# Kernel tuning notes

Measured on AMD Instinct MI355X. Metric: run time of the kernel, lower is better.

## Reference

```python
import jax, jax.numpy as jnp
import numpy as np

B, N, T, N_IN = 4, 40, 64, 4
N_EMB, N_HID = 32, 64
EPS = 1e-05


def _spatial_rels(n):
    # fully-connected directed edges without self-loops (NRI convention)
    offdiag = np.ones((n, n)) - np.eye(n)
    recv_idx, send_idx = np.where(offdiag)[0], np.where(offdiag)[1]
    eye = np.eye(n, dtype=np.float32)
    return eye[recv_idx], eye[send_idx]  # [n*(n-1), n] each


def _temporal_rels(t):
    # all t*t ordered pairs (including self), one-hot
    eye = np.eye(t, dtype=np.float32)
    recv = np.repeat(np.arange(t), t)
    send = np.tile(np.arange(t), t)
    return eye[recv], eye[send]  # [t*t, t] each


def setup_inputs() -> dict:
    key = jax.random.key(0)
    ks = jax.random.split(key, 8)
    rel_rec, rel_send = _spatial_rels(N)
    rel_rec_t, rel_send_t = _temporal_rels(T)
    s_emb = 1.0 / np.sqrt(N_IN)
    s_lstm = 1.0 / np.sqrt(N_HID)
    s_att = 1.0 / np.sqrt(2 * N_HID)
    return {
        "inputs": jax.random.normal(ks[0], (B, N, T, N_IN), dtype=jnp.float32),
        "rel_rec": jnp.asarray(rel_rec),
        "rel_send": jnp.asarray(rel_send),
        "rel_rec_t": jnp.asarray(rel_rec_t),
        "rel_send_t": jnp.asarray(rel_send_t),
        "W_emb": jax.random.uniform(ks[1], (N_EMB, N_IN), jnp.float32, -s_emb, s_emb),
        "b_emb": jnp.zeros((N_EMB,), jnp.float32),
        "W_ih": jax.random.uniform(ks[2], (4 * N_HID, N_EMB), jnp.float32, -s_lstm, s_lstm),
        "W_hh": jax.random.uniform(ks[3], (4 * N_HID, N_HID), jnp.float32, -s_lstm, s_lstm),
        "b_ih": jax.random.uniform(ks[4], (4 * N_HID,), jnp.float32, -s_lstm, s_lstm),
        "b_hh": jax.random.uniform(ks[5], (4 * N_HID,), jnp.float32, -s_lstm, s_lstm),
        "W_att": jax.random.uniform(ks[6], (1, 2 * N_HID), jnp.float32, -s_att, s_att),
        "b_att": jnp.zeros((1,), jnp.float32),
    }


def _forward(inputs, rel_rec, rel_send, rel_rec_t, rel_send_t,
             W_emb, b_emb, W_ih, W_hh, b_ih, b_hh, W_att, b_att):
    b, n, t, _ = inputs.shape
    nh = W_hh.shape[1]
    locs = inputs[..., :2]

    # ---- LSTMEncoder: per-timestep embedding + LSTM cell (scan over time) ----
    emb = jnp.einsum("bnti,ei->bnte", inputs, W_emb) + b_emb       # [B,N,T,n_emb]
    xs = emb.transpose(2, 0, 1, 3).reshape(t, b * n, -1)            # [T,BN,n_emb]

    def step(carry, x):
        h, c = carry
        gates = x @ W_ih.T + b_ih + h @ W_hh.T + b_hh               # [BN,4H]
        i_g, f_g, g_g, o_g = jnp.split(gates, 4, axis=-1)           # torch gate order i,f,g,o
        i_g = jax.nn.sigmoid(i_g)
        f_g = jax.nn.sigmoid(f_g)
        g_g = jnp.tanh(g_g)
        o_g = jax.nn.sigmoid(o_g)
        c = f_g * c + i_g * g_g
        h = o_g * jnp.tanh(c)
        return (h, c), h

    h0 = jnp.zeros((b * n, nh), inputs.dtype)
    _, hs_t = jax.lax.scan(step, (h0, h0), xs)                      # [T,BN,H]
    hs = hs_t.transpose(1, 0, 2).reshape(b, n, t, nh)               # [B,N,T,H]

    # ---- SoftAttention over timesteps ----
    hsf = hs.reshape(b * n, t, nh)                                  # [BN,T,H]
    senders = jnp.einsum("kt,mth->mkh", rel_send_t, hsf)            # [BN,T*T,H]
    receivers = jnp.einsum("kt,mth->mkh", rel_rec_t, hsf)
    edges = jnp.concatenate([senders, receivers], axis=-1)          # [BN,T*T,2H]
    scores = jnp.einsum("mkf,of->mko", edges, W_att)[..., 0] + b_att[0]  # [BN,T*T]
    # adj = rel_send_t^T @ diag(scores) @ rel_rec_t (done without diag_embed)
    adj_s = jnp.einsum("ki,mk,kj->mij", rel_send_t, scores, rel_rec_t)   # [BN,T,T]
    adj_sn = jax.nn.softmax(adj_s, axis=-1)
    cs = jnp.einsum("mij,mjh->mih", adj_sn, hsf).reshape(b, n, t, nh)    # [B,N,T,H]

    # ---- HardwiredAttention over atoms ----
    locs_re = locs.reshape(b, n, -1)                                 # [B,N,T*2]
    snd = jnp.einsum("en,bnf->bef", rel_send, locs_re).reshape(b, -1, t, 2)
    rcv = jnp.einsum("en,bnf->bef", rel_rec, locs_re).reshape(b, -1, t, 2)
    dist = jnp.sqrt(((snd - rcv) ** 2).sum(-1))                      # [B,E,T]
    w = (1.0 / (dist + EPS)).transpose(0, 2, 1)                      # [B,T,E]
    adj_h = jnp.einsum("ei,bte,ej->btij", rel_send, w, rel_rec)      # [B,T,N,N]
    ch = jnp.einsum("btij,btjh->btih", adj_h, hs.transpose(0, 2, 1, 3))
    ch = ch.transpose(0, 2, 1, 3)                                    # [B,N,T,H]

    c_out = jnp.tanh(jnp.concatenate([cs[:, :, -1, :], ch.sum(2)], axis=-1))  # [B,N,2H]
    return c_out


def reference(inputs, rel_rec, rel_send, rel_rec_t, rel_send_t,
              W_emb, b_emb, W_ih, W_hh, b_ih, b_hh, W_att, b_att):
    return _forward(inputs, rel_rec, rel_send, rel_rec_t, rel_send_t,
                    W_emb, b_emb, W_ih, W_hh, b_ih, b_hh, W_att, b_att)
```

## Files before the change

### kernel.cpp

```cpp
#include <hip/hip_runtime.h>
#include <math.h>

#define BB   4
#define NN   40
#define TT   64
#define NIN  4
#define NEMB 32
#define NHID 64
#define NG   256
#define EPSW 1e-5f

__device__ __align__(16) float g_hs[BB * NN * TT * NHID];

__device__ __forceinline__ float fast_sigmoid(float x) {
    return __fdividef(1.0f, 1.0f + __expf(-x));
}
__device__ __forceinline__ float fast_tanh(float x) {
    return __fdividef(2.0f, 1.0f + __expf(-2.0f * x)) - 1.0f;
}
__device__ __forceinline__ float lanebcast(float v, int l) {
    return __int_as_float(__builtin_amdgcn_readlane(__float_as_int(v), l));
}

__global__ __launch_bounds__(256, 1)
void k_lstm(const float* __restrict__ inputs,
            const float* __restrict__ W_emb,
            const float* __restrict__ b_emb,
            const float* __restrict__ W_ih,
            const float* __restrict__ W_hh,
            const float* __restrict__ b_ih,
            const float* __restrict__ b_hh,
            const float* __restrict__ W_att,
            float* __restrict__ out)
{
    __shared__ __align__(16) float s_x[TT * NIN];
    __shared__ __align__(16) float s_act[2][NG];
    __shared__ __align__(16) float s_hs[TT * (NHID + 1)];
    __shared__ __align__(16) float s_war[NHID];
    __shared__ __align__(16) float s_p[TT];

    const int m   = blockIdx.x;
    const int tid = threadIdx.x;
    const int g   = tid;
    const int j   = tid & 63;
    const int gtype = g >> 6;

    s_x[tid] = inputs[m * (TT * NIN) + tid];
    if (tid < NHID) s_war[tid] = W_att[NHID + tid];

    float wcx = 0.f, wcy = 0.f, wcz = 0.f, wcw = 0.f;
    float bc  = b_ih[g] + b_hh[g];
    {
        const float4* wih4  = (const float4*)(W_ih + g * NEMB);
        const float4* wemb4 = (const float4*)W_emb;
        #pragma unroll
        for (int e4 = 0; e4 < NEMB / 4; ++e4) {
            float4 wv = wih4[e4];
            float4 m0 = wemb4[4 * e4 + 0];
            float4 m1 = wemb4[4 * e4 + 1];
            float4 m2 = wemb4[4 * e4 + 2];
            float4 m3 = wemb4[4 * e4 + 3];
            wcx += wv.x * m0.x + wv.y * m1.x + wv.z * m2.x + wv.w * m3.x;
            wcy += wv.x * m0.y + wv.y * m1.y + wv.z * m2.y + wv.w * m3.y;
            wcz += wv.x * m0.z + wv.y * m1.z + wv.z * m2.z + wv.w * m3.z;
            wcw += wv.x * m0.w + wv.y * m1.w + wv.z * m2.w + wv.w * m3.w;
            bc  += wv.x * b_emb[4 * e4 + 0] + wv.y * b_emb[4 * e4 + 1]
                 + wv.z * b_emb[4 * e4 + 2] + wv.w * b_emb[4 * e4 + 3];
        }
    }

    const float4* q4 = (const float4*)(W_hh + g * NHID);
    float4 w0 = q4[0],  w1 = q4[1],  w2 = q4[2],  w3 = q4[3];
    float4 w4 = q4[4],  w5 = q4[5],  w6 = q4[6],  w7 = q4[7];
    float4 w8 = q4[8],  w9 = q4[9],  wA = q4[10], wB = q4[11];
    float4 wC = q4[12], wD = q4[13], wE = q4[14], wF = q4[15];
    #define PIN4(W) asm volatile("" : "+v"(W.x), "+v"(W.y), "+v"(W.z), "+v"(W.w))
    PIN4(w0); PIN4(w1); PIN4(w2); PIN4(w3);
    PIN4(w4); PIN4(w5); PIN4(w6); PIN4(w7);
    PIN4(w8); PIN4(w9); PIN4(wA); PIN4(wB);
    PIN4(wC); PIN4(wD); PIN4(wE); PIN4(wF);
    #undef PIN4

    __syncthreads();

    float c = 0.0f, h = 0.0f;
    #pragma unroll 1
    for (int t = 0; t < TT; ++t) {
        const int p = t & 1;
        const float4 x = ((const float4*)s_x)[t];

        float v0 = bc, v1 = 0.f, v2 = 0.f, v3 = 0.f;
        #define DOT4(W, K) {                                  \
            v0 += lanebcast(h, 4*(K)+0) * W.x;                \
            v1 += lanebcast(h, 4*(K)+1) * W.y;                \
            v2 += lanebcast(h, 4*(K)+2) * W.z;                \
            v3 += lanebcast(h, 4*(K)+3) * W.w; }
        DOT4(w0, 0)  DOT4(w1, 1)  DOT4(w2, 2)  DOT4(w3, 3)
        DOT4(w4, 4)  DOT4(w5, 5)  DOT4(w6, 6)  DOT4(w7, 7)
        DOT4(w8, 8)  DOT4(w9, 9)  DOT4(wA, 10) DOT4(wB, 11)
        DOT4(wC, 12) DOT4(wD, 13) DOT4(wE, 14) DOT4(wF, 15)
        #undef DOT4
        const float vx = x.x * wcx + x.y * wcy + x.z * wcz + x.w * wcw;
        const float v  = ((v0 + v1) + (v2 + v3)) + vx;

        const float a = (gtype == 2) ? fast_tanh(v) : fast_sigmoid(v);
        s_act[p][g] = a;
        __syncthreads();

        const float ig = s_act[p][j];
        const float fg = s_act[p][NHID + j];
        const float gg = s_act[p][2 * NHID + j];
        const float og = s_act[p][3 * NHID + j];
        c = fg * c + ig * gg;
        h = og * fast_tanh(c);
        if (gtype == 0) s_hs[t * (NHID + 1) + j] = h;
    }
    __syncthreads();

    #pragma unroll
    for (int idx = tid; idx < TT * NHID; idx += 256) {
        const int t = idx >> 6, hh = idx & 63;
        g_hs[m * (TT * NHID) + idx] = s_hs[t * (NHID + 1) + hh];
    }

    if (tid < TT) {
        const int t = tid;
        float r = 0.0f;
        #pragma unroll
        for (int k = 0; k < NHID; ++k)
            r += s_hs[t * (NHID + 1) + k] * s_war[k];
        float mx = r;
        #pragma unroll
        for (int off = 32; off >= 1; off >>= 1)
            mx = fmaxf(mx, __shfl_xor(mx, off));
        const float e = __expf(r - mx);
        float s = e;
        #pragma unroll
        for (int off = 32; off >= 1; off >>= 1)
            s += __shfl_xor(s, off);
        s_p[t] = __fdividef(e, s);
    }
    __syncthreads();

    if (tid < NHID) {
        float acc = 0.0f;
        #pragma unroll
        for (int t = 0; t < TT; ++t)
            acc += s_p[t] * s_hs[t * (NHID + 1) + tid];
        out[m * (2 * NHID) + tid] = fast_tanh(acc);
    }
}

__global__ __launch_bounds__(1024)
void k_spatial(const float* __restrict__ inputs,
               float* __restrict__ out)
{
    __shared__ float s_w[TT * NN];
    __shared__ float s_part[16 * NHID];

    const int bi  = blockIdx.x;
    const int b   = bi / NN;
    const int i   = bi - b * NN;
    const int tid = threadIdx.x;

    for (int idx = tid; idx < TT * NN; idx += 1024) {
        const int t = idx / NN;
        const int j = idx - t * NN;
        const float* pi = inputs + ((b * NN + i) * TT + t) * NIN;
        const float* pj = inputs + ((b * NN + j) * TT + t) * NIN;
        const float dx = pi[0] - pj[0];
        const float dy = pi[1] - pj[1];
        const float d  = sqrtf(dx * dx + dy * dy);
        s_w[idx] = (j == i) ? 0.0f : __fdividef(1.0f, d + EPSW);
    }
    __syncthreads();

    const int h = tid & 63;
    const int q = tid >> 6;

    const float* base = g_hs + (size_t)b * NN * TT * NHID + h;
    float a0 = 0.f, a1 = 0.f, a2 = 0.f, a3 = 0.f;
    for (int t = q * 4; t < q * 4 + 4; ++t) {
        const float* hp = base + t * NHID;
        const float* wp = s_w + t * NN;
        #pragma unroll
        for (int j = 0; j < NN; j += 4) {
            a0 += wp[j + 0] * hp[(size_t)(j + 0) * TT * NHID];
            a1 += wp[j + 1] * hp[(size_t)(j + 1) * TT * NHID];
            a2 += wp[j + 2] * hp[(size_t)(j + 2) * TT * NHID];
            a3 += wp[j + 3] * hp[(size_t)(j + 3) * TT * NHID];
        }
    }
    s_part[q * NHID + h] = (a0 + a1) + (a2 + a3);
    __syncthreads();

    if (tid < NHID) {
        float s = 0.f;
        #pragma unroll
        for (int q2 = 0; q2 < 16; ++q2)
            s += s_part[q2 * NHID + tid];
        out[bi * (2 * NHID) + NHID + tid] = fast_tanh(s);
    }
}

extern "C" void kernel_launch(void* const* d_in, const int* in_sizes, int n_in,
                              void* d_out, int out_size, void* d_ws, size_t ws_size,
                              hipStream_t stream) {
    const float* inputs = (const float*)d_in[0];
    const float* W_emb  = (const float*)d_in[5];
    const float* b_emb  = (const float*)d_in[6];
    const float* W_ih   = (const float*)d_in[7];
    const float* W_hh   = (const float*)d_in[8];
    const float* b_ih   = (const float*)d_in[9];
    const float* b_hh   = (const float*)d_in[10];
    const float* W_att  = (const float*)d_in[11];
    (void)d_ws; (void)ws_size;

    float* outp = (float*)d_out;

    hipLaunchKernelGGL(k_lstm, dim3(BB * NN), dim3(256), 0, stream,
                       inputs, W_emb, b_emb, W_ih, W_hh, b_ih, b_hh, W_att,
                       outp);
    hipLaunchKernelGGL(k_spatial, dim3(BB * NN), dim3(1024), 0, stream,
                       inputs, outp);
}
```

Measured before the change: 129.6 us.

## Pack two LSTM sequences per workgroup and drop register pinning

The LSTM kernel now processes two (batch, node) sequences per 512-thread workgroup, halving the grid to 80 blocks, with all shared buffers duplicated per sequence. The inline-asm register pins on the W_hh weights are also removed, leaving allocation to the compiler. The intent is to reduce workgroup count and launch overhead, but the per-step __syncthreads now couples two independent recurrences. Only 80 of the GPU's compute units would be busy instead of 160, so the serial 64-step recurrence may take longer per block.

```diff
diff --git a/kernel.cpp b/kernel.cpp
--- a/kernel.cpp
+++ b/kernel.cpp
@@ -22,7 +22,7 @@
     return __int_as_float(__builtin_amdgcn_readlane(__float_as_int(v), l));
 }
 
-__global__ __launch_bounds__(256, 1)
+__global__ __launch_bounds__(512, 1)
 void k_lstm(const float* __restrict__ inputs,
             const float* __restrict__ W_emb,
             const float* __restrict__ b_emb,
@@ -33,19 +33,21 @@
             const float* __restrict__ W_att,
             float* __restrict__ out)
 {
-    __shared__ __align__(16) float s_x[TT * NIN];
-    __shared__ __align__(16) float s_act[2][NG];
-    __shared__ __align__(16) float s_hs[TT * (NHID + 1)];
+    __shared__ __align__(16) float s_x[2][TT * NIN];
+    __shared__ __align__(16) float s_act[2][2][NG];
+    __shared__ __align__(16) float s_hs[2][TT * (NHID + 1)];
     __shared__ __align__(16) float s_war[NHID];
-    __shared__ __align__(16) float s_p[TT];
-
-    const int m   = blockIdx.x;
+    __shared__ __align__(16) float s_p[2][TT];
+
     const int tid = threadIdx.x;
-    const int g   = tid;
-    const int j   = tid & 63;
-    const int gtype = g >> 6;
-
-    s_x[tid] = inputs[m * (TT * NIN) + tid];
+    const int s   = tid >> 8;
+    const int tl  = tid & 255;
+    const int m   = blockIdx.x * 2 + s;
+    const int g   = tl;
+    const int j   = tl & 63;
+    const int gtype = tl >> 6;
+
+    s_x[s][tl] = inputs[m * (TT * NIN) + tl];
     if (tid < NHID) s_war[tid] = W_att[NHID + tid];
 
     float wcx = 0.f, wcy = 0.f, wcz = 0.f, wcw = 0.f;
@@ -74,12 +76,6 @@
     float4 w4 = q4[4],  w5 = q4[5],  w6 = q4[6],  w7 = q4[7];
     float4 w8 = q4[8],  w9 = q4[9],  wA = q4[10], wB = q4[11];
     float4 wC = q4[12], wD = q4[13], wE = q4[14], wF = q4[15];
-    #define PIN4(W) asm volatile("" : "+v"(W.x), "+v"(W.y), "+v"(W.z), "+v"(W.w))
-    PIN4(w0); PIN4(w1); PIN4(w2); PIN4(w3);
-    PIN4(w4); PIN4(w5); PIN4(w6); PIN4(w7);
-    PIN4(w8); PIN4(w9); PIN4(wA); PIN4(wB);
-    PIN4(wC); PIN4(wD); PIN4(wE); PIN4(wF);
-    #undef PIN4
 
     __syncthreads();
 
@@ -87,7 +83,7 @@
     #pragma unroll 1
     for (int t = 0; t < TT; ++t) {
         const int p = t & 1;
-        const float4 x = ((const float4*)s_x)[t];
+        const float4 x = ((const float4*)s_x[s])[t];
 
         float v0 = bc, v1 = 0.f, v2 = 0.f, v3 = 0.f;
         #define DOT4(W, K) {                                  \
@@ -104,50 +100,50 @@
         const float v  = ((v0 + v1) + (v2 + v3)) + vx;
 
         const float a = (gtype == 2) ? fast_tanh(v) : fast_sigmoid(v);
-        s_act[p][g] = a;
+        s_act[s][p][g] = a;
         __syncthreads();
 
-        const float ig = s_act[p][j];
-        const float fg = s_act[p][NHID + j];
-        const float gg = s_act[p][2 * NHID + j];
-        const float og = s_act[p][3 * NHID + j];
+        const float ig = s_act[s][p][j];
+        const float fg = s_act[s][p][NHID + j];
+        const float gg = s_act[s][p][2 * NHID + j];
+        const float og = s_act[s][p][3 * NHID + j];
         c = fg * c + ig * gg;
         h = og * fast_tanh(c);
-        if (gtype == 0) s_hs[t * (NHID + 1) + j] = h;
+        if (gtype == 0) s_hs[s][t * (NHID + 1) + j] = h;
     }
     __syncthreads();
 
     #pragma unroll
-    for (int idx = tid; idx < TT * NHID; idx += 256) {
+    for (int idx = tl; idx < TT * NHID; idx += 256) {
         const int t = idx >> 6, hh = idx & 63;
-        g_hs[m * (TT * NHID) + idx] = s_hs[t * (NHID + 1) + hh];
-    }
-
-    if (tid < TT) {
-        const int t = tid;
+        g_hs[m * (TT * NHID) + idx] = s_hs[s][t * (NHID + 1) + hh];
+    }
+
+    if (tl < TT) {
+        const int t = tl;
         float r = 0.0f;
         #pragma unroll
         for (int k = 0; k < NHID; ++k)
-            r += s_hs[t * (NHID + 1) + k] * s_war[k];
+            r += s_hs[s][t * (NHID + 1) + k] * s_war[k];
         float mx = r;
         #pragma unroll
         for (int off = 32; off >= 1; off >>= 1)
             mx = fmaxf(mx, __shfl_xor(mx, off));
         const float e = __expf(r - mx);
-        float s = e;
+        float sm = e;
         #pragma unroll
         for (int off = 32; off >= 1; off >>= 1)
-            s += __shfl_xor(s, off);
-        s_p[t] = __fdividef(e, s);
-    }
-    __syncthreads();
-
-    if (tid < NHID) {
+            sm += __shfl_xor(sm, off);
+        s_p[s][t] = __fdividef(e, sm);
+    }
+    __syncthreads();
+
+    if (tl < NHID) {
         float acc = 0.0f;
         #pragma unroll
         for (int t = 0; t < TT; ++t)
-            acc += s_p[t] * s_hs[t * (NHID + 1) + tid];
-        out[m * (2 * NHID) + tid] = fast_tanh(acc);
+            acc += s_p[s][t] * s_hs[s][t * (NHID + 1) + tl];
+        out[m * (2 * NHID) + tl] = fast_tanh(acc);
     }
 }
 
@@ -218,7 +214,7 @@
 
     float* outp = (float*)d_out;
 
-    hipLaunchKernelGGL(k_lstm, dim3(BB * NN), dim3(256), 0, stream,
+    hipLaunchKernelGGL(k_lstm, dim3(BB * NN / 2), dim3(512), 0, stream,
                        inputs, W_emb, b_emb, W_ih, W_hh, b_ih, b_hh, W_att,
                        outp);
     hipLaunchKernelGGL(k_spatial, dim3(BB * NN), dim3(1024), 0, stream,
```

New measurement: 148.4 us. +14.5%, slower.
